# Kernel optimization log

Measured on AMD Instinct MI355X. Metric: run time of the kernel, lower is better.

## Reference

```python
import jax, jax.numpy as jnp
import numpy as np

N_CLASS = 50257
EMB = 1024
HID = 1024
BATCH = 1024  # must equal HID due to the module's [H,H] zero state init
SEQ = 128


def setup_inputs() -> dict:
    key = jax.random.key(0)
    ks = jax.random.split(key, 8)
    s_e = 1.0 / np.sqrt(EMB)
    s_h = 1.0 / np.sqrt(HID)
    X = jax.random.randint(ks[0], (BATCH, SEQ), 0, N_CLASS, dtype=jnp.int32)
    C = jax.random.normal(ks[1], (N_CLASS, EMB), dtype=jnp.float32)
    # gate order along last axis: i, f, g, o (each block of size HID)
    Wx = jax.random.uniform(ks[2], (EMB, 4 * HID), jnp.float32, -s_e, s_e)
    bx = jax.random.uniform(ks[3], (4 * HID,), jnp.float32, -s_e, s_e)
    Wh = jax.random.uniform(ks[4], (HID, 4 * HID), jnp.float32, -s_h, s_h)
    bh = jax.random.uniform(ks[5], (4 * HID,), jnp.float32, -s_h, s_h)
    W_out = jax.random.uniform(ks[6], (HID, N_CLASS), jnp.float32, -s_h, s_h)
    b_out = jnp.ones((N_CLASS,), dtype=jnp.float32)  # nn.Parameter(torch.ones)
    return {"X": X, "C": C, "Wx": Wx, "bx": bx, "Wh": Wh, "bh": bh,
            "W_out": W_out, "b_out": b_out}


def _lstm_last_hidden(xs, Wx, bx, Wh, bh):
    # xs: [S, B, E]; with zero-initialized h/c of shape [H,H] and B == H,
    # the original broadcast-buggy code reduces to a standard LSTM.
    x_proj = jnp.einsum('sbe,eg->sbg', xs, Wx) + bx  # [S, B, 4H]
    B = xs.shape[1]
    H = Wh.shape[0]
    h0 = jnp.zeros((B, H), dtype=xs.dtype)
    c0 = jnp.zeros((B, H), dtype=xs.dtype)

    def step(carry, xp):
        h, c = carry
        gates = xp + h @ Wh + bh  # [B, 4H]
        i, f, g, o = jnp.split(gates, 4, axis=-1)
        i = jax.nn.sigmoid(i)
        f = jax.nn.sigmoid(f)
        g = jnp.tanh(g)
        o = jax.nn.sigmoid(o)
        c = f * c + i * g
        h = o * jnp.tanh(c)
        return (h, c), None

    (h, _), _ = jax.lax.scan(step, (h0, c0), x_proj)
    return h  # [B, H] last timestep hidden


def reference(X, C, Wx, bx, Wh, bh, W_out, b_out):
    emb = C[X]                      # [B, S, E]
    xs = jnp.swapaxes(emb, 0, 1)    # [S, B, E]  (transpose(0,1))
    h_last = _lstm_last_hidden(xs, Wx, bx, Wh, bh)
    return h_last @ W_out + b_out   # [B, n_class]
```

## Files before the change

kernel.cpp:

```cpp
#include <hip/hip_runtime.h>
#include <hip/hip_bf16.h>

#define SEQ_   128
#define NCLS_  50257
#define EMB_   1024
#define HID_   1024
#define BATCH_ 1024
#define G4_    4096

typedef __attribute__((ext_vector_type(8))) short short8;
typedef __attribute__((ext_vector_type(4))) float f32x4;

__device__ __forceinline__ void async_copy16(void* lds, const void* g) {
  __builtin_amdgcn_global_load_lds(
      (const __attribute__((address_space(1))) void*)g,
      (__attribute__((address_space(3))) void*)lds, 16, 0, 0);
}

__device__ __forceinline__ void mfma_acc(f32x4& c, const short8& a, const short8& b) {
  asm("v_mfma_f32_16x16x32_bf16 %0, %1, %2, %0" : "+v"(c) : "v"(a), "v"(b));
}

__device__ __forceinline__ float sigmoidf_(float x) {
  return 1.f / (1.f + __expf(-x));
}
__device__ __forceinline__ float tanhf_(float x) {
  x = fminf(12.f, fmaxf(-12.f, x));
  float e = __expf(2.f * x);
  return (e - 1.f) / (e + 1.f);
}
__device__ __forceinline__ float bf2f_(ushort u) {
  return __uint_as_float(((unsigned int)u) << 16);
}

template <int EPI>
__global__ __launch_bounds__(512) void gemm8p(
    const __hip_bfloat16* __restrict__ A,
    const __hip_bfloat16* __restrict__ Bt,
    float* __restrict__ outF, __hip_bfloat16* __restrict__ outB,
    int Mreal, int Nreal, long ostride, const float* __restrict__ bias0) {
  extern __shared__ __align__(16) char smem[];

  const int tid = threadIdx.x;
  const int lane = tid & 63;
  const int w = tid >> 6;
  const int wm = w >> 2;
  const int wn = w & 3;
  const int m0 = blockIdx.y * 128;
  const int n0 = blockIdx.x * 256;

  const int fr = lane & 15;
  const int kb = (lane >> 4) * 16;
  const int swz = (fr & 7) << 4;

  f32x4 acc[4][4];
#pragma unroll
  for (int i = 0; i < 4; ++i)
#pragma unroll
    for (int j = 0; j < 4; ++j) acc[i][j] = (f32x4)(0.0f);

  auto STAGE3 = [&](int kc, int part) {
    const int slot = kc % 3;
#pragma unroll
    for (int q = 0; q < 3; ++q) {
      const int inst = part * 3 + q;
      char* dst;
      const __hip_bfloat16* src;
      if (inst < 2) {
        const int r = inst * 512 + tid;
        const int row = r >> 3, ch = r & 7;
        long ar = m0 + row; if (ar >= Mreal) ar = Mreal - 1;
        src = A + ar * 1024 + kc * 64 + ch * 8;
        dst = smem + slot * 49152 + r * 16;
      } else {
        const int r = (inst - 2) * 512 + tid;
        const int row = r >> 3, ch = r & 7;
        long br = n0 + row; if (br >= Nreal) br = Nreal - 1;
        src = Bt + br * 1024 + kc * 64 + ch * 8;
        dst = smem + slot * 49152 + 16384 + r * 16;
      }
      async_copy16(dst, src);
    }
  };

  STAGE3(0, 0); STAGE3(0, 1);
  STAGE3(1, 0); STAGE3(1, 1);
  asm volatile("s_waitcnt vmcnt(6)" ::: "memory");
  __builtin_amdgcn_s_barrier();

  for (int t = 0; t < 16; ++t) {
    const char* baseA = smem + (t % 3) * 49152;
    const char* baseB = baseA + 16384;
#pragma unroll
    for (int kk = 0; kk < 2; ++kk) {
      if (t + 2 < 16) STAGE3(t + 2, kk);
      __builtin_amdgcn_sched_barrier(0);

      short8 aR[4], bR[4];
#pragma unroll
      for (int f = 0; f < 4; ++f) {
        aR[f] = *(const short8*)(baseA + (wm * 64 + f * 16 + fr) * 128 +
                                 ((kk * 64 + kb) ^ swz));
        bR[f] = *(const short8*)(baseB + (wn * 64 + f * 16 + fr) * 128 +
                                 ((kk * 64 + kb) ^ swz));
      }
      __builtin_amdgcn_s_barrier();
      asm volatile("s_waitcnt lgkmcnt(0)" ::: "memory");
      __builtin_amdgcn_sched_barrier(0);
      __builtin_amdgcn_s_setprio(1);
#pragma unroll
      for (int fm = 0; fm < 4; ++fm)
#pragma unroll
        for (int fn = 0; fn < 4; ++fn)
          mfma_acc(acc[fm][fn], aR[fm], bR[fn]);
      __builtin_amdgcn_s_setprio(0);
      __builtin_amdgcn_sched_barrier(0);
      if (kk == 1) {
        if (t < 14)       asm volatile("s_waitcnt vmcnt(6)" ::: "memory");
        else if (t == 14) asm volatile("s_waitcnt vmcnt(0)" ::: "memory");
      }
      __builtin_amdgcn_s_barrier();
    }
  }

  const int cn = lane & 15;
  const int rb = (lane >> 4) * 4;
#pragma unroll
  for (int fn = 0; fn < 4; ++fn) {
    const int col = n0 + wn * 64 + fn * 16 + cn;
    const float badd = (EPI == 0) ? bias0[col]
                                  : ((col < Nreal) ? bias0[col] : 0.f);
#pragma unroll
    for (int fm = 0; fm < 4; ++fm) {
#pragma unroll
      for (int r = 0; r < 4; ++r) {
        const int row = m0 + wm * 64 + fm * 16 + rb + r;
        const float v = acc[fm][fn][r] + badd;
        if (EPI == 0) {
          if (row < Mreal) outB[(long)row * ostride + col] = __float2bfloat16(v);
        } else {
          if (col < Nreal) outF[(long)row * ostride + col] = v;
        }
      }
    }
  }
}

__global__ __launch_bounds__(256) void pack_b(const float* __restrict__ Wh,
                                              __hip_bfloat16* __restrict__ Bpk) {
  const int gtid = blockIdx.x * 256 + threadIdx.x;
  const int l = gtid & 63;
  const int tile = gtid >> 6;
  const int g = tile & 3;
  const int kk = (tile >> 2) & 1;
  const int kc = (tile >> 3) & 7;
  const int kh = (tile >> 6) & 1;
  const int wn = (tile >> 7) & 1;
  const int ht = tile >> 8;
  const int h = ht * 32 + wn * 16 + (l & 15);
  const int k0 = kh * 512 + kc * 64 + kk * 32 + (l >> 4) * 8;
  short8 v;
#pragma unroll
  for (int e = 0; e < 8; ++e) {
    const __hip_bfloat16 b = __float2bfloat16(Wh[(size_t)(k0 + e) * G4_ + g * 1024 + h]);
    v[e] = *reinterpret_cast<const short*>(&b);
  }
  *(short8*)(Bpk + (size_t)gtid * 8) = v;
}

__global__ __launch_bounds__(512, 2) void lstm_step(
    const __hip_bfloat16* __restrict__ hprev,
    const __hip_bfloat16* __restrict__ Bpk,
    const __hip_bfloat16* __restrict__ Epr,
    const int* __restrict__ X,
    float* __restrict__ cbuf,
    __hip_bfloat16* __restrict__ hnext,
    __hip_bfloat16* __restrict__ hfin,
    int t, int last) {
  extern __shared__ __align__(16) char smem[];
  float* gacc = (float*)smem;

  const int tid = threadIdx.x;
  const int lane = tid & 63;
  const int w = tid >> 6;
  const int wm = (w >> 1) & 1;
  const int wn = w & 1;
  const int kh = w >> 2;
  const int bid = blockIdx.x;
  const int xcd = bid & 7;
  const int j = bid >> 3;
  const int ht = xcd * 4 + (j & 3);
  const int mt = j >> 2;
  const int m0 = mt * 128;
  const int h0 = ht * 32;

  const int fr = lane & 15;
  const int kb = (lane >> 4) * 16;
  const int swz = (fr & 7) << 4;
  const int cn = lane & 15;
  const int rb = (lane >> 4) * 4;

  const int crow = tid >> 2;
  const int hq = tid & 3;
  const int prow = m0 + crow;
  const int tok1 = X[prow * SEQ_ + t];

  const __hip_bfloat16* bb =
      Bpk + (size_t)(((ht * 2 + wn) * 2 + kh) * 64) * 512 + lane * 8;

  f32x4 acc[4][4];
#pragma unroll
  for (int i = 0; i < 4; ++i)
#pragma unroll
    for (int g = 0; g < 4; ++g) acc[i][g] = (f32x4)(0.0f);

  auto STAGE_A = [&](int kc, int b) {
#pragma unroll
    for (int q = 0; q < 4; ++q) {
      const int region = q >> 1;
      const int r = (q & 1) * 512 + tid;
      const int row = r >> 3, ch = r & 7;
      const __hip_bfloat16* src =
          hprev + (size_t)(m0 + row) * HID_ + region * 512 + kc * 64 + ch * 8;
      async_copy16(smem + b * 32768 + region * 16384 + r * 16, src);
    }
  };

  short8 bR[2][2][4];

  STAGE_A(0, 0);
#pragma unroll
  for (int kk = 0; kk < 2; ++kk)
#pragma unroll
    for (int g = 0; g < 4; ++g)
      bR[0][kk][g] = *(const short8*)(bb + (0 * 8 + kk * 4 + g) * 512);
  STAGE_A(1, 1);

#pragma unroll
  for (int kc = 0; kc < 8; ++kc) {
    __builtin_amdgcn_s_barrier();
    if (kc + 1 < 8) {
#pragma unroll
      for (int kk = 0; kk < 2; ++kk)
#pragma unroll
        for (int g = 0; g < 4; ++g)
          bR[(kc + 1) & 1][kk][g] =
              *(const short8*)(bb + ((kc + 1) * 8 + kk * 4 + g) * 512);
    }
    if (kc + 2 < 8) STAGE_A(kc + 2, (kc + 2) % 3);
    if (kc < 6)      asm volatile("s_waitcnt vmcnt(24)" ::: "memory");
    else if (kc == 6) asm volatile("s_waitcnt vmcnt(20)" ::: "memory");
    else             asm volatile("s_waitcnt vmcnt(8)" ::: "memory");
    __builtin_amdgcn_sched_barrier(0);

    const char* baseA = smem + (kc % 3) * 32768 + kh * 16384;
    short8 aR[2][4];
#pragma unroll
    for (int kk = 0; kk < 2; ++kk)
#pragma unroll
      for (int f = 0; f < 4; ++f)
        aR[kk][f] = *(const short8*)(baseA + (wm * 64 + f * 16 + fr) * 128 +
                                     ((kk * 64 + kb) ^ swz));
    __builtin_amdgcn_s_setprio(1);
#pragma unroll
    for (int fm = 0; fm < 4; ++fm)
#pragma unroll
      for (int g = 0; g < 4; ++g) {
        mfma_acc(acc[fm][g], aR[0][fm], bR[kc & 1][0][g]);
        mfma_acc(acc[fm][g], aR[1][fm], bR[kc & 1][1][g]);
      }
    __builtin_amdgcn_s_setprio(0);
  }

  ushort4 ep[8];
  float cold[8];
#pragma unroll
  for (int jj = 0; jj < 8; ++jj) {
    ep[jj] = *(const ushort4*)(Epr + (size_t)tok1 * G4_ + (h0 + hq * 8 + jj) * 4);
    cold[jj] = cbuf[(size_t)prow * HID_ + h0 + hq * 8 + jj];
  }

  __syncthreads();
  if (kh == 0) {
#pragma unroll
    for (int fm = 0; fm < 4; ++fm)
#pragma unroll
      for (int g = 0; g < 4; ++g)
#pragma unroll
        for (int r = 0; r < 4; ++r)
          gacc[(wm * 64 + fm * 16 + rb + r) * 132 + (wn * 16 + cn) * 4 + g] =
              acc[fm][g][r];
  }
  __syncthreads();
  if (kh == 1) {
#pragma unroll
    for (int fm = 0; fm < 4; ++fm)
#pragma unroll
      for (int g = 0; g < 4; ++g)
#pragma unroll
        for (int r = 0; r < 4; ++r)
          gacc[(wm * 64 + fm * 16 + rb + r) * 132 + (wn * 16 + cn) * 4 + g] +=
              acc[fm][g][r];
  }
  __syncthreads();

  const float* gr = gacc + crow * 132 + hq * 32;
  f32x4 cnew0, cnew1;
  short8 hv;
#pragma unroll
  for (int jj = 0; jj < 8; ++jj) {
    const f32x4 g4 = *(const f32x4*)(gr + jj * 4);
    const float iv = sigmoidf_(g4[0] + bf2f_(ep[jj].x));
    const float fv = sigmoidf_(g4[1] + bf2f_(ep[jj].y));
    const float gv = tanhf_(g4[2] + bf2f_(ep[jj].z));
    const float ov = sigmoidf_(g4[3] + bf2f_(ep[jj].w));
    const float cv = fv * cold[jj] + iv * gv;
    if (jj < 4) cnew0[jj] = cv; else cnew1[jj - 4] = cv;
    const float hval = ov * tanhf_(cv);
    const __hip_bfloat16 hb = __float2bfloat16(hval);
    hv[jj] = *reinterpret_cast<const short*>(&hb);
  }
  float* cdst = cbuf + (size_t)prow * HID_ + h0 + hq * 8;
  *(f32x4*)cdst = cnew0;
  *(f32x4*)(cdst + 4) = cnew1;
  const int hcolb = h0 + hq * 8;
  const int hswb = (hcolb & ~63) | ((hcolb & 63) ^ ((prow & 7) << 3));
  *(short8*)(hnext + (size_t)prow * HID_ + hswb) = hv;
  if (last) *(short8*)(hfin + (size_t)prow * HID_ + hswb) = hv;
}

template <bool SWZ>
__global__ __launch_bounds__(256) void conv_bf16_k(const float* __restrict__ in,
                                                   __hip_bfloat16* __restrict__ out, int n4) {
  const int i = blockIdx.x * 256 + threadIdx.x;
  if (i >= n4) return;
  const float4 v = ((const float4*)in)[i];
  int o = i * 4;
  if (SWZ) {
    const int row = o >> 10, col = o & 1023;
    const int cs = (col & ~63) | ((col & 63) ^ ((row & 7) << 3));
    o = (o & ~1023) | cs;
  }
  out[o + 0] = __float2bfloat16(v.x);
  out[o + 1] = __float2bfloat16(v.y);
  out[o + 2] = __float2bfloat16(v.z);
  out[o + 3] = __float2bfloat16(v.w);
}

template <bool PERM, bool SWZ>
__global__ __launch_bounds__(256) void transpose_conv(const float* __restrict__ in,
                                                      __hip_bfloat16* __restrict__ out,
                                                      int R, int C) {
  __shared__ float tile[32][33];
  const int c0 = blockIdx.x * 32, r0 = blockIdx.y * 32;
  const int tx = threadIdx.x, ty = threadIdx.y;
#pragma unroll
  for (int i = 0; i < 4; ++i) {
    const int r = r0 + ty + i * 8, cc = c0 + tx;
    tile[ty + i * 8][tx] = (r < R && cc < C) ? in[(size_t)r * C + cc] : 0.f;
  }
  __syncthreads();
#pragma unroll
  for (int i = 0; i < 4; ++i) {
    const int ro = c0 + ty + i * 8, co = r0 + tx;
    if (ro < C && co < R) {
      const int n = PERM ? ((ro & 1023) * 4 + (ro >> 10)) : ro;
      int k = co;
      if (SWZ) k = (k & ~63) | ((k & 63) ^ ((n & 7) << 3));
      out[(size_t)n * R + k] = __float2bfloat16(tile[tx][ty + i * 8]);
    }
  }
}

__global__ __launch_bounds__(256) void bias_perm(const float* __restrict__ bx,
                                                 const float* __restrict__ bh,
                                                 float* __restrict__ bP) {
  const int n = blockIdx.x * 256 + threadIdx.x;
  if (n >= G4_) return;
  const int h = n >> 2, g = n & 3;
  bP[n] = bx[g * HID_ + h] + bh[g * HID_ + h];
}

extern "C" void kernel_launch(void* const* d_in, const int* in_sizes, int n_in,
                              void* d_out, int out_size, void* d_ws, size_t ws_size,
                              hipStream_t stream) {
  const int* X = (const int*)d_in[0];
  const float* C = (const float*)d_in[1];
  const float* Wx = (const float*)d_in[2];
  const float* bx = (const float*)d_in[3];
  const float* Wh = (const float*)d_in[4];
  const float* bh = (const float*)d_in[5];
  const float* Wo = (const float*)d_in[6];
  const float* bo = (const float*)d_in[7];
  float* out = (float*)d_out;

  char* p = (char*)d_ws;
  const size_t szCb  = (size_t)NCLS_ * EMB_ * 2;
  const size_t szWxt = (size_t)G4_ * EMB_ * 2;
  const size_t szBpk = (size_t)G4_ * HID_ * 2;
  const size_t szEpr = (size_t)NCLS_ * G4_ * 2;
  const size_t szH   = (size_t)BATCH_ * HID_ * 2;
  const size_t szC   = (size_t)BATCH_ * HID_ * 4;
  const size_t szBp  = (size_t)G4_ * 4;
  if (ws_size < szCb + szWxt + szBpk + szEpr + 3 * szH + szC + szBp) return;

  __hip_bfloat16* Cb   = (__hip_bfloat16*)p; p += szCb;
  __hip_bfloat16* WxtP = (__hip_bfloat16*)p; p += szWxt;
  __hip_bfloat16* Bpk  = (__hip_bfloat16*)p; p += szBpk;
  __hip_bfloat16* Epr  = (__hip_bfloat16*)p; p += szEpr;
  __hip_bfloat16* hA   = (__hip_bfloat16*)p; p += szH;
  __hip_bfloat16* hB   = (__hip_bfloat16*)p; p += szH;
  __hip_bfloat16* hfin = (__hip_bfloat16*)p; p += szH;
  float* cbuf          = (float*)p;          p += szC;
  float* bP            = (float*)p;          p += szBp;

  {
    const int n4 = NCLS_ * EMB_ / 4;
    conv_bf16_k<true><<<(n4 + 255) / 256, 256, 0, stream>>>(C, Cb, n4);
  }
  transpose_conv<true, true><<<dim3(G4_ / 32, EMB_ / 32), dim3(32, 8), 0, stream>>>(
      Wx, WxtP, EMB_, G4_);
  pack_b<<<2048, 256, 0, stream>>>(Wh, Bpk);
  bias_perm<<<G4_ / 256, 256, 0, stream>>>(bx, bh, bP);

  gemm8p<0><<<dim3(G4_ / 256, (NCLS_ + 127) / 128), 512, 147456, stream>>>(
      Cb, WxtP, nullptr, Epr, NCLS_, G4_, G4_, bP);

  hipMemsetAsync(hA, 0, szH, stream);
  hipMemsetAsync(cbuf, 0, szC, stream);

  for (int t = 0; t < SEQ_; ++t) {
    const __hip_bfloat16* hp = (t & 1) ? hB : hA;
    __hip_bfloat16* hn = (t & 1) ? hA : hB;
    lstm_step<<<256, 512, 98304, stream>>>(hp, Bpk, Epr, X, cbuf, hn, hfin, t,
                                           (int)(t == SEQ_ - 1));
  }

  __hip_bfloat16* Wot = Cb;
  transpose_conv<false, true><<<dim3((NCLS_ + 31) / 32, HID_ / 32), dim3(32, 8), 0,
                                stream>>>(Wo, Wot, HID_, NCLS_);

  gemm8p<2><<<dim3((NCLS_ + 255) / 256, BATCH_ / 128), 512, 147456, stream>>>(
      hfin, Wot, out, nullptr, BATCH_, NCLS_, NCLS_, bo);
}
```

Measured before the change: 3.168 ms.

## Enlarge GEMM tiles to 256x256 with double-buffered LDS pipeline

The bf16 MFMA GEMM now uses 256x256 output tiles, with each wave computing 128x64 instead of 64x64, so each LDS-loaded tile is reused more often. The three-stage split-load pipeline is replaced by a simpler two-buffer scheme: the next K-chunk is prefetched whole, followed by a wait and one barrier per chunk. This raises arithmetic intensity and cuts barrier count, but doubles accumulator registers (likely lowering occupancy), makes prefetch overlap coarser, and gives fewer blocks for the 1024-row output GEMM.

```diff
diff --git a/kernel.cpp b/kernel.cpp
--- a/kernel.cpp
+++ b/kernel.cpp
@@ -34,7 +34,7 @@
 }
 
 template <int EPI>
-__global__ __launch_bounds__(512) void gemm8p(
+__global__ __launch_bounds__(512) void gemm256sq(
     const __hip_bfloat16* __restrict__ A,
     const __hip_bfloat16* __restrict__ Bt,
     float* __restrict__ outF, __hip_bfloat16* __restrict__ outB,
@@ -46,81 +46,73 @@
   const int w = tid >> 6;
   const int wm = w >> 2;
   const int wn = w & 3;
-  const int m0 = blockIdx.y * 128;
+  const int m0 = blockIdx.y * 256;
   const int n0 = blockIdx.x * 256;
 
   const int fr = lane & 15;
   const int kb = (lane >> 4) * 16;
   const int swz = (fr & 7) << 4;
 
-  f32x4 acc[4][4];
-#pragma unroll
-  for (int i = 0; i < 4; ++i)
+  f32x4 acc[8][4];
+#pragma unroll
+  for (int i = 0; i < 8; ++i)
 #pragma unroll
     for (int j = 0; j < 4; ++j) acc[i][j] = (f32x4)(0.0f);
 
-  auto STAGE3 = [&](int kc, int part) {
-    const int slot = kc % 3;
-#pragma unroll
-    for (int q = 0; q < 3; ++q) {
-      const int inst = part * 3 + q;
+  auto STAGE = [&](int kc, int b) {
+#pragma unroll
+    for (int q = 0; q < 8; ++q) {
+      const int r = (q & 3) * 512 + tid;
+      const int row = r >> 3;
+      const int ch = r & 7;
+      const __hip_bfloat16* src;
       char* dst;
-      const __hip_bfloat16* src;
-      if (inst < 2) {
-        const int r = inst * 512 + tid;
-        const int row = r >> 3, ch = r & 7;
+      if (q < 4) {
         long ar = m0 + row; if (ar >= Mreal) ar = Mreal - 1;
         src = A + ar * 1024 + kc * 64 + ch * 8;
-        dst = smem + slot * 49152 + r * 16;
+        dst = smem + b * 65536 + r * 16;
       } else {
-        const int r = (inst - 2) * 512 + tid;
-        const int row = r >> 3, ch = r & 7;
         long br = n0 + row; if (br >= Nreal) br = Nreal - 1;
         src = Bt + br * 1024 + kc * 64 + ch * 8;
-        dst = smem + slot * 49152 + 16384 + r * 16;
+        dst = smem + b * 65536 + 32768 + r * 16;
       }
       async_copy16(dst, src);
     }
   };
 
-  STAGE3(0, 0); STAGE3(0, 1);
-  STAGE3(1, 0); STAGE3(1, 1);
-  asm volatile("s_waitcnt vmcnt(6)" ::: "memory");
-  __builtin_amdgcn_s_barrier();
-
-  for (int t = 0; t < 16; ++t) {
-    const char* baseA = smem + (t % 3) * 49152;
-    const char* baseB = baseA + 16384;
+  STAGE(0, 0);
+  for (int kc = 0; kc < 16; ++kc) {
+    const int b = kc & 1;
+    if (kc + 1 < 16) {
+      STAGE(kc + 1, b ^ 1);
+      asm volatile("s_waitcnt vmcnt(8)" ::: "memory");
+    } else {
+      asm volatile("s_waitcnt vmcnt(0)" ::: "memory");
+    }
+    __builtin_amdgcn_s_barrier();
+    __builtin_amdgcn_sched_barrier(0);
+
 #pragma unroll
     for (int kk = 0; kk < 2; ++kk) {
-      if (t + 2 < 16) STAGE3(t + 2, kk);
-      __builtin_amdgcn_sched_barrier(0);
-
-      short8 aR[4], bR[4];
-#pragma unroll
-      for (int f = 0; f < 4; ++f) {
-        aR[f] = *(const short8*)(baseA + (wm * 64 + f * 16 + fr) * 128 +
-                                 ((kk * 64 + kb) ^ swz));
-        bR[f] = *(const short8*)(baseB + (wn * 64 + f * 16 + fr) * 128 +
-                                 ((kk * 64 + kb) ^ swz));
-      }
-      __builtin_amdgcn_s_barrier();
-      asm volatile("s_waitcnt lgkmcnt(0)" ::: "memory");
-      __builtin_amdgcn_sched_barrier(0);
+      short8 aR[8], bR[4];
+#pragma unroll
+      for (int f = 0; f < 8; ++f)
+        aR[f] = *(const short8*)(smem + b * 65536 +
+                 (wm * 128 + f * 16 + fr) * 128 + ((kk * 64 + kb) ^ swz));
+#pragma unroll
+      for (int f = 0; f < 4; ++f)
+        bR[f] = *(const short8*)(smem + b * 65536 + 32768 +
+                 (wn * 64 + f * 16 + fr) * 128 + ((kk * 64 + kb) ^ swz));
       __builtin_amdgcn_s_setprio(1);
 #pragma unroll
-      for (int fm = 0; fm < 4; ++fm)
+      for (int fm = 0; fm < 8; ++fm)
 #pragma unroll
         for (int fn = 0; fn < 4; ++fn)
           mfma_acc(acc[fm][fn], aR[fm], bR[fn]);
       __builtin_amdgcn_s_setprio(0);
-      __builtin_amdgcn_sched_barrier(0);
-      if (kk == 1) {
-        if (t < 14)       asm volatile("s_waitcnt vmcnt(6)" ::: "memory");
-        else if (t == 14) asm volatile("s_waitcnt vmcnt(0)" ::: "memory");
-      }
-      __builtin_amdgcn_s_barrier();
-    }
+    }
+    __builtin_amdgcn_sched_barrier(0);
+    __builtin_amdgcn_s_barrier();
   }
 
   const int cn = lane & 15;
@@ -131,15 +123,15 @@
     const float badd = (EPI == 0) ? bias0[col]
                                   : ((col < Nreal) ? bias0[col] : 0.f);
 #pragma unroll
-    for (int fm = 0; fm < 4; ++fm) {
+    for (int fm = 0; fm < 8; ++fm) {
 #pragma unroll
       for (int r = 0; r < 4; ++r) {
-        const int row = m0 + wm * 64 + fm * 16 + rb + r;
+        const int row = m0 + wm * 128 + fm * 16 + rb + r;
         const float v = acc[fm][fn][r] + badd;
         if (EPI == 0) {
           if (row < Mreal) outB[(long)row * ostride + col] = __float2bfloat16(v);
         } else {
-          if (col < Nreal) outF[(long)row * ostride + col] = v;
+          if (col < Nreal && row < Mreal) outF[(long)row * ostride + col] = v;
         }
       }
     }
@@ -423,7 +415,7 @@
   pack_b<<<2048, 256, 0, stream>>>(Wh, Bpk);
   bias_perm<<<G4_ / 256, 256, 0, stream>>>(bx, bh, bP);
 
-  gemm8p<0><<<dim3(G4_ / 256, (NCLS_ + 127) / 128), 512, 147456, stream>>>(
+  gemm256sq<0><<<dim3(G4_ / 256, (NCLS_ + 255) / 256), 512, 131072, stream>>>(
       Cb, WxtP, nullptr, Epr, NCLS_, G4_, G4_, bP);
 
   hipMemsetAsync(hA, 0, szH, stream);
@@ -440,6 +432,6 @@
   transpose_conv<false, true><<<dim3((NCLS_ + 31) / 32, HID_ / 32), dim3(32, 8), 0,
                                 stream>>>(Wo, Wot, HID_, NCLS_);
 
-  gemm8p<2><<<dim3((NCLS_ + 255) / 256, BATCH_ / 128), 512, 147456, stream>>>(
+  gemm256sq<2><<<dim3((NCLS_ + 255) / 256, BATCH_ / 256), 512, 131072, stream>>>(
       hfin, Wot, out, nullptr, BATCH_, NCLS_, NCLS_, bo);
 }
```

New measurement: 3.212 ms. About the same (+1.4%).
